# Performance work log

Measured on AMD Instinct MI355X. Metric: run time of the kernel, lower is better.

Reference implementation:

```python
import jax, jax.numpy as jnp
import numpy as np

B, L, D, H = 2, 2048, 1024, 16
HD = D // H
ROPE_BASE = 10000.0


def _chain_info(lengths):
    """lengths: [B, L] int, chain lengths packed at the front, zeros after.
    Returns per-position within-chain positions (RoPE resets per chain),
    chain ids, and a validity mask."""
    def one(row):
        csum = jnp.cumsum(row)                      # [L]
        total = csum[-1]
        p = jnp.arange(L)
        cid = jnp.searchsorted(csum, p, side='right')  # chain id per position
        prev = jnp.where(cid > 0, csum[jnp.clip(cid - 1, 0, L - 1)], 0)
        valid = p < total
        pos = jnp.where(valid, p - prev, 0).astype(jnp.float32)
        return pos, cid, valid
    return jax.vmap(one)(lengths)


def _rope_tables(pos):
    # pos: [B, L] float -> cos/sin [B, L, 1, HD]
    inv_freq = 1.0 / (ROPE_BASE ** (jnp.arange(0, HD, 2, dtype=jnp.float32) / HD))
    freqs = pos[..., None] * inv_freq               # [B, L, HD/2]
    emb = jnp.concatenate([freqs, freqs], axis=-1)  # [B, L, HD]
    return jnp.cos(emb)[:, :, None, :], jnp.sin(emb)[:, :, None, :]


def _apply_rope(x, cos, sin):
    d = x.shape[-1]
    x1, x2 = x[..., : d // 2], x[..., d // 2:]
    return x * cos + jnp.concatenate([-x2, x1], axis=-1) * sin


def _branch(x, Wqkv, bqkv, cos, sin, allowed):
    # x: [B, L, D]; allowed: [B, L, L] bool attention mask for this branch
    qkv = x @ Wqkv.T + bqkv                          # [B, L, 3D]
    qkv = qkv.reshape(B, L, 3, H, HD)
    q, k, v = qkv[:, :, 0], qkv[:, :, 1], qkv[:, :, 2]
    q = q * (HD ** -0.5)
    q = _apply_rope(q, cos, sin)
    k = _apply_rope(k, cos, sin)
    scores = jnp.einsum('bthd,bshd->bhts', q, k)     # [B, H, L, L]
    scores = jnp.where(allowed[:, None], scores, -jnp.inf)
    probs = jax.nn.softmax(scores, axis=-1)
    probs = jnp.where(jnp.isnan(probs), 0.0, probs)  # fully-masked rows -> 0
    out = jnp.einsum('bhts,bshd->bthd', probs, v)    # [B, L, H, HD]
    return out.reshape(B, L, D)


def setup_inputs() -> dict:
    key = jax.random.key(0)
    ks = jax.random.split(key, 7)
    s = 0.02
    lens = np.zeros((B, L), np.int64)
    lens[0, :8] = [300, 250, 200, 400, 350, 248, 150, 100]   # sum 1998
    lens[1, :6] = [512, 400, 300, 360, 276, 200]             # sum 2048
    return {
        'hidden_states': jax.random.normal(ks[0], (B, L, D), jnp.float32),
        'attention_mask_in_length': jnp.asarray(lens),
        'Wqkv_intra': jax.random.normal(ks[1], (3 * D, D), jnp.float32) * s,
        'bqkv_intra': jnp.zeros((3 * D,), jnp.float32),
        'Wqkv_inter': jax.random.normal(ks[2], (3 * D, D), jnp.float32) * s,
        'bqkv_inter': jnp.zeros((3 * D,), jnp.float32),
        'Wout': jax.random.normal(ks[3], (D, D), jnp.float32) * s,
        'bout': jnp.zeros((D,), jnp.float32),
    }


def reference(hidden_states, attention_mask_in_length, Wqkv_intra, bqkv_intra,
              Wqkv_inter, bqkv_inter, Wout, bout):
    pos, cid, valid = _chain_info(attention_mask_in_length)
    cos, sin = _rope_tables(pos)
    same_chain = cid[:, :, None] == cid[:, None, :]          # [B, L, L]
    key_valid = valid[:, None, :]                            # [B, 1, L]
    allowed_intra = same_chain & key_valid
    allowed_inter = (~same_chain) & key_valid
    out_intra = _branch(hidden_states, Wqkv_intra, bqkv_intra, cos, sin, allowed_intra)
    out_inter = _branch(hidden_states, Wqkv_inter, bqkv_inter, cos, sin, allowed_inter)
    return (out_intra + out_inter) @ Wout.T + bout
```

## Files before the change

### kernel.cpp

```cpp
#include <hip/hip_runtime.h>
#include <hip/hip_bf16.h>
#include <stdint.h>

#define B 2
#define L 2048
#define D 1024
#define H 16
#define HD 64
#define NT (L / 64)
#define NQT (L / 128)
#define INVALID_CID 0x40000000
#define BHLHD ((size_t)B * H * L * HD)

typedef __hip_bfloat16 bf16;
typedef __attribute__((ext_vector_type(8))) short short8;
typedef __attribute__((ext_vector_type(4))) float floatx4;
typedef __attribute__((ext_vector_type(4))) unsigned int uint4v;

static __device__ __forceinline__ short f2bf(float f) {
    bf16 h = __float2bfloat16(f);
    return *reinterpret_cast<short*>(&h);
}

static __device__ __forceinline__ void async_copy16(const void* g, void* l) {
    __builtin_amdgcn_global_load_lds((__attribute__((address_space(1))) void*)g,
                                     (__attribute__((address_space(3))) void*)l,
                                     16, 0, 0);
}

__global__ void chain_kernel(const int* __restrict__ lens,
                             float* __restrict__ pos, int* __restrict__ cid,
                             int4* __restrict__ tinfo)
{
    __shared__ int csum[L];
    __shared__ int cids[L];
    __shared__ int part[256];
    int b = blockIdx.x;
    int t = threadIdx.x;

    int loc[8];
    int s = 0;
    #pragma unroll
    for (int j = 0; j < 8; ++j) { s += lens[b * L + t * 8 + j]; loc[j] = s; }
    part[t] = s;
    __syncthreads();
    if (t == 0) {
        int acc = 0;
        for (int i = 0; i < 256; ++i) { int v = part[i]; part[i] = acc; acc += v; }
    }
    __syncthreads();
    int base = part[t];
    #pragma unroll
    for (int j = 0; j < 8; ++j) csum[t * 8 + j] = base + loc[j];
    __syncthreads();

    int total = csum[L - 1];
    for (int p = t; p < L; p += 256) {
        int cv;
        if (p < total) {
            int lo = 0, hi = L;
            while (lo < hi) {
                int mid = (lo + hi) >> 1;
                if (csum[mid] <= p) lo = mid + 1; else hi = mid;
            }
            int prev = (lo > 0) ? csum[lo - 1] : 0;
            pos[b * L + p] = (float)(p - prev);
            cv = lo;
        } else {
            pos[b * L + p] = 0.f;
            cv = INVALID_CID;
        }
        cids[p] = cv;
        cid[b * L + p] = cv;
    }
    __syncthreads();
    if (t < NT) {
        int mn = 0x7fffffff, mx = -1, any = 0, all = 1;
        for (int j = 0; j < 64; ++j) {
            int cv = cids[t * 64 + j];
            if (cv != INVALID_CID) { any = 1; mn = min(mn, cv); mx = max(mx, cv); }
            else all = 0;
        }
        tinfo[b * NT + t] = make_int4(mn, mx, any | (all << 1), 0);
    }
}

__global__ void rope_table(const float* __restrict__ pos, float2* __restrict__ tab)
{
    int idx = blockIdx.x * 256 + threadIdx.x;
    int j = idx & 31, l = idx >> 5;
    float invf = exp2f(-(float)j * (13.287712379549449f / 32.f));
    float ang = pos[l] * invf;
    tab[idx] = make_float2(cosf(ang), sinf(ang));
}

__global__ void cast_all(const float* __restrict__ x,  const float* __restrict__ Wi,
                         const float* __restrict__ We, const float* __restrict__ Wo,
                         bf16* __restrict__ xb, bf16* __restrict__ Wib,
                         bf16* __restrict__ Web, bf16* __restrict__ Wob)
{
    int bid = blockIdx.x;
    const float* src; bf16* dst; int base;
    if      (bid < 4096)  { src = x;  dst = xb;  base = bid; }
    else if (bid < 7168)  { src = Wi; dst = Wib; base = bid - 4096; }
    else if (bid < 10240) { src = We; dst = Web; base = bid - 7168; }
    else                  { src = Wo; dst = Wob; base = bid - 10240; }
    int i = (base * 256 + threadIdx.x) * 4;
    float4 v = *(const float4*)(src + i);
    dst[i + 0] = __float2bfloat16(v.x);
    dst[i + 1] = __float2bfloat16(v.y);
    dst[i + 2] = __float2bfloat16(v.z);
    dst[i + 3] = __float2bfloat16(v.w);
}

__global__ __launch_bounds__(256, 4) void gemm_qkv(
    const bf16* __restrict__ A, const bf16* __restrict__ Bw,
    const float* __restrict__ bi, const float* __restrict__ be,
    const float2* __restrict__ tab,
    bf16* __restrict__ Qo, bf16* __restrict__ Ko, bf16* __restrict__ Vto)
{
    __shared__ short Smem[2 * 128 * 32];
    short* As = Smem;
    short* Bs = Smem + 128 * 32;

    int tid = threadIdx.x;
    int wave = tid >> 6, lane = tid & 63;
    int i15 = lane & 15, q8 = lane >> 4;
    int wm = wave & 1, wn = wave >> 1;
    int m0 = blockIdx.y * 128, n0 = blockIdx.x * 128;
    const int K = D;

    floatx4 acc[4][4];
    #pragma unroll
    for (int mt = 0; mt < 4; ++mt)
        #pragma unroll
        for (int nt = 0; nt < 4; ++nt) acc[mt][nt] = (floatx4){0.f, 0.f, 0.f, 0.f};

    const short* gA = (const short*)A  + (size_t)(m0 + wave * 32 + (lane >> 2)) * K + (lane & 3) * 8;
    const short* gB = (const short*)Bw + (size_t)(n0 + wave * 32 + (lane >> 2)) * K + (lane & 3) * 8;
    short* lA = As + wave * 1024;
    short* lB = Bs + wave * 1024;

    for (int kt = 0; kt < K; kt += 32) {
        __syncthreads();
        async_copy16(gA + kt,          lA);
        async_copy16(gA + 16 * K + kt, lA + 512);
        async_copy16(gB + kt,          lB);
        async_copy16(gB + 16 * K + kt, lB + 512);
        __syncthreads();

        short8 af[4], bfr[4];
        #pragma unroll
        for (int mt = 0; mt < 4; ++mt)
            af[mt] = *(const short8*)&As[(wm * 64 + mt * 16 + i15) * 32 + q8 * 8];
        #pragma unroll
        for (int nt = 0; nt < 4; ++nt)
            bfr[nt] = *(const short8*)&Bs[(wn * 64 + nt * 16 + i15) * 32 + q8 * 8];
        #pragma unroll
        for (int mt = 0; mt < 4; ++mt)
            #pragma unroll
            for (int nt = 0; nt < 4; ++nt)
                acc[mt][nt] = __builtin_amdgcn_mfma_f32_16x16x32_bf16(af[mt], bfr[nt], acc[mt][nt], 0, 0, 0);
    }

    int nb = n0 + wn * 64;
    int segw = nb >> 10;
    int br = (segw >= 3);
    int st = segw - 3 * br;
    int h = (nb >> 6) & (H - 1);
    int b = m0 >> 11;
    int lb = (m0 & (L - 1)) + wm * 64;

    float bv[4];
    #pragma unroll
    for (int nt = 0; nt < 4; ++nt) {
        int n = nb + nt * 16 + i15;
        bv[nt] = (n < 3 * D) ? bi[n] : be[n - 3 * D];
    }

    if (st != 2) {
        bf16* out = (st == 0 ? Qo : Ko) + (size_t)br * BHLHD;
        const size_t bh = (size_t)(b * H + h) * L;
        float qs = (st == 0) ? 0.18033688011111772f : 1.0f;
        #pragma unroll
        for (int mt = 0; mt < 4; ++mt) {
            #pragma unroll
            for (int rg = 0; rg < 4; ++rg) {
                int m = m0 + wm * 64 + mt * 16 + q8 * 4 + rg;
                int l = lb + mt * 16 + q8 * 4 + rg;
                float2 cs0 = tab[(size_t)m * 32 + i15];
                float2 cs1 = tab[(size_t)m * 32 + 16 + i15];
                size_t orow = (bh + l) * HD;
                #pragma unroll
                for (int nt = 0; nt < 4; ++nt) {
                    float x  = acc[mt][nt][rg] + bv[nt];
                    float pr = acc[mt][nt ^ 2][rg] + bv[nt ^ 2];
                    float cc = (nt & 1) ? cs1.x : cs0.x;
                    float ss = (nt & 1) ? cs1.y : cs0.y;
                    float v = qs * (x * cc + ((nt < 2) ? -pr : pr) * ss);
                    out[orow + nt * 16 + i15] = __float2bfloat16(v);
                }
            }
        }
    } else {
        bf16* out = Vto + (size_t)br * BHLHD;
        const size_t bhd = (size_t)(b * H + h) * HD;
        __syncthreads();
        short* vts = Smem + wave * 64 * 20;
        #pragma unroll
        for (int mt = 0; mt < 4; ++mt) {
            #pragma unroll
            for (int nt = 0; nt < 4; ++nt) {
                uint2 w;
                w.x = (unsigned)(unsigned short)f2bf(acc[mt][nt][0] + bv[nt]) |
                      ((unsigned)(unsigned short)f2bf(acc[mt][nt][1] + bv[nt]) << 16);
                w.y = (unsigned)(unsigned short)f2bf(acc[mt][nt][2] + bv[nt]) |
                      ((unsigned)(unsigned short)f2bf(acc[mt][nt][3] + bv[nt]) << 16);
                *(uint2*)&vts[(nt * 16 + i15) * 20 + q8 * 4] = w;
            }
            uint2 r0 = *(const uint2*)&vts[lane * 20 + 0];
            uint2 r1 = *(const uint2*)&vts[lane * 20 + 4];
            uint2 r2 = *(const uint2*)&vts[lane * 20 + 8];
            uint2 r3 = *(const uint2*)&vts[lane * 20 + 12];
            size_t ga = (bhd + lane) * L + lb + mt * 16;
            uint4v v0 = (uint4v){r0.x, r0.y, r1.x, r1.y};
            uint4v v1 = (uint4v){r2.x, r2.y, r3.x, r3.y};
            *(uint4v*)&out[ga]     = v0;
            *(uint4v*)&out[ga + 8] = v1;
        }
    }
}

__global__ __launch_bounds__(256, 4) void gemm128(
    const bf16* __restrict__ A, const bf16* __restrict__ Bw,
    const float* __restrict__ bias, void* __restrict__ Cout,
    int M, int N, int K, int c_bf16)
{
    __shared__ short As[128 * 32];
    __shared__ short Bs[128 * 32];

    int tid = threadIdx.x;
    int wave = tid >> 6, lane = tid & 63;
    int i15 = lane & 15, q8 = lane >> 4;
    int wm = wave & 1, wn = wave >> 1;
    int m0 = blockIdx.y * 128, n0 = blockIdx.x * 128;

    floatx4 acc[4][4];
    #pragma unroll
    for (int mt = 0; mt < 4; ++mt)
        #pragma unroll
        for (int nt = 0; nt < 4; ++nt) acc[mt][nt] = (floatx4){0.f, 0.f, 0.f, 0.f};

    const short* gA = (const short*)A  + (size_t)(m0 + wave * 32 + (lane >> 2)) * K + (lane & 3) * 8;
    const short* gB = (const short*)Bw + (size_t)(n0 + wave * 32 + (lane >> 2)) * K + (lane & 3) * 8;
    short* lA = As + wave * 1024;
    short* lB = Bs + wave * 1024;

    for (int kt = 0; kt < K; kt += 32) {
        __syncthreads();
        async_copy16(gA + kt,          lA);
        async_copy16(gA + 16 * K + kt, lA + 512);
        async_copy16(gB + kt,          lB);
        async_copy16(gB + 16 * K + kt, lB + 512);
        __syncthreads();

        short8 af[4], bfr[4];
        #pragma unroll
        for (int mt = 0; mt < 4; ++mt)
            af[mt] = *(const short8*)&As[(wm * 64 + mt * 16 + i15) * 32 + q8 * 8];
        #pragma unroll
        for (int nt = 0; nt < 4; ++nt)
            bfr[nt] = *(const short8*)&Bs[(wn * 64 + nt * 16 + i15) * 32 + q8 * 8];
        #pragma unroll
        for (int mt = 0; mt < 4; ++mt)
            #pragma unroll
            for (int nt = 0; nt < 4; ++nt)
                acc[mt][nt] = __builtin_amdgcn_mfma_f32_16x16x32_bf16(af[mt], bfr[nt], acc[mt][nt], 0, 0, 0);
    }

    #pragma unroll
    for (int nt = 0; nt < 4; ++nt) {
        int n = n0 + wn * 64 + nt * 16 + i15;
        float bv = bias[n];
        #pragma unroll
        for (int mt = 0; mt < 4; ++mt) {
            #pragma unroll
            for (int rg = 0; rg < 4; ++rg) {
                int m = m0 + wm * 64 + mt * 16 + q8 * 4 + rg;
                float v = acc[mt][nt][rg] + bv;
                if (c_bf16) ((bf16*)Cout)[(size_t)m * N + n] = __float2bfloat16(v);
                else        ((float*)Cout)[(size_t)m * N + n] = v;
            }
        }
    }
}

__global__ __launch_bounds__(256, 2) void attn7(
    const bf16* __restrict__ Qg, const bf16* __restrict__ Kgg, const bf16* __restrict__ Vtgg,
    const int* __restrict__ cid, const int4* __restrict__ tinfo,
    bf16* __restrict__ Out)
{
    __shared__ short Ks[2][64][72];
    __shared__ short Vs[2][64][72];
    __shared__ int cls0_s[NT], cls1_s[NT];
    __shared__ int list_s[2][NT];
    __shared__ int nlist_s[2];

    int tid = threadIdx.x;
    int wave = tid >> 6, lane = tid & 63;
    int i15 = lane & 15, q8 = lane >> 4;
    int workid = ((blockIdx.x & 7) << 6) | (blockIdx.x >> 3);
    int qt = workid & (NQT - 1);
    int h  = (workid >> 4) & (H - 1);
    int b  = workid >> 8;
    int q0 = qt * 128;
    const size_t bh  = (size_t)(b * H + h) * L;
    const size_t bhd = (size_t)(b * H + h) * HD;

    int cq[2];
    #pragma unroll
    for (int g = 0; g < 2; ++g)
        cq[g] = cid[b * L + q0 + g * 64 + wave * 16 + i15];

    int4 qa = tinfo[b * NT + 2 * qt];
    int4 qb4 = tinfo[b * NT + 2 * qt + 1];
    int4 qinf;
    qinf.x = min(qa.x, qb4.x);
    qinf.y = max(qa.y, qb4.y);
    qinf.z = ((qa.z | qb4.z) & 1) | (qa.z & qb4.z & 2);
    int qall = (qinf.z >> 1) & 1;

    if (tid < NT) {
        int4 ki = tinfo[b * NT + tid];
        int kany = ki.z & 1, kall = (ki.z >> 1) & 1;
        bool disjoint = (ki.x > qinf.y) || (ki.y < qinf.x);
        bool mono = qall && kall && (qinf.x == qinf.y) && (ki.x == ki.y) && (qinf.x == ki.x);
        cls0_s[tid] = (!kany || disjoint) ? 0 : (mono ? 2 : 1);
        cls1_s[tid] = (!kany || mono) ? 0 : ((kall && disjoint) ? 2 : 1);
    }
    __syncthreads();
    if (tid < 2) {
        const int* cls = tid ? cls1_s : cls0_s;
        int n = 0;
        for (int t = 0; t < NT; ++t) {
            int c = cls[t];
            if (c) list_s[tid][n++] = (t * 64) | ((c == 2) << 16);
        }
        nlist_s[tid] = n;
    }
    __syncthreads();

    int r = tid >> 2, ccol = (tid & 3) * 16;
    int sr = ((((r >> 2) & 1) | ((r >> 5) << 1)) << 4) | (((r >> 3) & 3) << 2) | (r & 3);

    floatx4 accO[2][2][4];
    #pragma unroll
    for (int br = 0; br < 2; ++br)
        #pragma unroll
        for (int g = 0; g < 2; ++g)
            #pragma unroll
            for (int t = 0; t < 4; ++t) accO[br][g][t] = (floatx4){0.f, 0.f, 0.f, 0.f};
    float lsum[2][2] = {{0.f, 0.f}, {0.f, 0.f}};

    #pragma unroll
    for (int br = 0; br < 2; ++br) {
        const short* Qb    = (const short*)Qg  + (size_t)br * BHLHD;
        const short* Kbase = (const short*)Kgg + (size_t)br * BHLHD + (bh + r) * HD + ccol;
        const short* Vbase = (const short*)Vtgg + (size_t)br * BHLHD + (bhd + r) * L + ccol;
        int n = nlist_s[br];

        short8 qf[2][2];
        #pragma unroll
        for (int g = 0; g < 2; ++g) {
            const short* qp = Qb + (bh + q0 + g * 64 + wave * 16 + i15) * HD + q8 * 8;
            qf[g][0] = *(const short8*)(qp);
            qf[g][1] = *(const short8*)(qp + 32);
        }

        int4 pk0, pk1, pv0, pv1;
        int cur = 0;
        if (n > 0) {
            cur = list_s[br][0];
            int kt0 = cur & 0xffff;
            pk0 = *(const int4*)(Kbase + (size_t)kt0 * HD);
            pk1 = *(const int4*)(Kbase + (size_t)kt0 * HD + 8);
            pv0 = *(const int4*)(Vbase + kt0);
            pv1 = *(const int4*)(Vbase + kt0 + 8);
        }
        __syncthreads();

        for (int i = 0; i < n; ++i) {
            int kt = cur & 0xffff, full = cur >> 16;
            int buf = i & 1;

            *(int4*)&Ks[buf][sr][ccol]     = pk0;
            *(int4*)&Ks[buf][sr][ccol + 8] = pk1;
            *(int4*)&Vs[buf][r][ccol]      = pv0;
            *(int4*)&Vs[buf][r][ccol + 8]  = pv1;
            __syncthreads();

            if (i + 1 < n) {
                cur = list_s[br][i + 1];
                int nk = cur & 0xffff;
                pk0 = *(const int4*)(Kbase + (size_t)nk * HD);
                pk1 = *(const int4*)(Kbase + (size_t)nk * HD + 8);
                pv0 = *(const int4*)(Vbase + nk);
                pv1 = *(const int4*)(Vbase + nk + 8);
            }

            unsigned int dl[2][4], dh[2][4];
            #pragma unroll
            for (int t = 0; t < 4; ++t) {
                short8 b0 = *(const short8*)&Ks[buf][t * 16 + i15][q8 * 8];
                short8 b1 = *(const short8*)&Ks[buf][t * 16 + i15][32 + q8 * 8];

                floatx4 accS[2];
                #pragma unroll
                for (int g = 0; g < 2; ++g) {
                    accS[g] = (floatx4){0.f, 0.f, 0.f, 0.f};
                    accS[g] = __builtin_amdgcn_mfma_f32_16x16x32_bf16(b0, qf[g][0], accS[g], 0, 0, 0);
                    accS[g] = __builtin_amdgcn_mfma_f32_16x16x32_bf16(b1, qf[g][1], accS[g], 0, 0, 0);
                }

                if (!full) {
                    int4 ck4 = *(const int4*)(cid + b * L + kt + (q8 << 3) + ((t & 1) << 2) + ((t >> 1) << 5));
                    int ckr[4] = {ck4.x, ck4.y, ck4.z, ck4.w};
                    #pragma unroll
                    for (int g = 0; g < 2; ++g)
                        #pragma unroll
                        for (int rg = 0; rg < 4; ++rg) {
                            bool kv = (ckr[rg] != INVALID_CID);
                            bool match = (cq[g] == ckr[rg]);
                            bool ok = kv && (br ? !match : match);
                            accS[g][rg] = ok ? accS[g][rg] : -1e30f;
                        }
                }

                #pragma unroll
                for (int g = 0; g < 2; ++g) {
                    float p0 = __builtin_amdgcn_exp2f(accS[g][0]);
                    float p1 = __builtin_amdgcn_exp2f(accS[g][1]);
                    float p2 = __builtin_amdgcn_exp2f(accS[g][2]);
                    float p3 = __builtin_amdgcn_exp2f(accS[g][3]);
                    lsum[br][g] += (p0 + p1) + (p2 + p3);
                    dl[g][t] = (unsigned)(unsigned short)f2bf(p0) | ((unsigned)(unsigned short)f2bf(p1) << 16);
                    dh[g][t] = (unsigned)(unsigned short)f2bf(p2) | ((unsigned)(unsigned short)f2bf(p3) << 16);
                }
            }

            union { uint4v u; short8 s; } pa0[2], pa1[2];
            #pragma unroll
            for (int g = 0; g < 2; ++g) {
                pa0[g].u = (uint4v){dl[g][0], dh[g][0], dl[g][1], dh[g][1]};
                pa1[g].u = (uint4v){dl[g][2], dh[g][2], dl[g][3], dh[g][3]};
            }

            #pragma unroll
            for (int dt = 0; dt < 4; ++dt) {
                short8 vf0 = *(const short8*)&Vs[buf][dt * 16 + i15][q8 * 8];
                short8 vf1 = *(const short8*)&Vs[buf][dt * 16 + i15][32 + q8 * 8];
                #pragma unroll
                for (int g = 0; g < 2; ++g) {
                    accO[br][g][dt] = __builtin_amdgcn_mfma_f32_16x16x32_bf16(pa0[g].s, vf0, accO[br][g][dt], 0, 0, 0);
                    accO[br][g][dt] = __builtin_amdgcn_mfma_f32_16x16x32_bf16(pa1[g].s, vf1, accO[br][g][dt], 0, 0, 0);
                }
            }
        }
    }

    float inv[2][2][4];
    #pragma unroll
    for (int br = 0; br < 2; ++br)
        #pragma unroll
        for (int g = 0; g < 2; ++g) {
            float ls = lsum[br][g];
            ls += __shfl_xor(ls, 16, 64);
            ls += __shfl_xor(ls, 32, 64);
            #pragma unroll
            for (int rg = 0; rg < 4; ++rg) {
                float lv = __shfl(ls, q8 * 4 + rg, 64);
                inv[br][g][rg] = (lv > 0.f) ? 1.f / lv : 0.f;
            }
        }

    #pragma unroll
    for (int g = 0; g < 2; ++g)
        #pragma unroll
        for (int t = 0; t < 4; ++t)
            #pragma unroll
            for (int rg = 0; rg < 4; ++rg) {
                size_t idx = (size_t)(b * L + q0 + g * 64 + wave * 16 + q8 * 4 + rg) * D + h * HD + t * 16 + i15;
                float o = accO[0][g][t][rg] * inv[0][g][rg] + accO[1][g][t][rg] * inv[1][g][rg];
                Out[idx] = __float2bfloat16(o);
            }
}

extern "C" void kernel_launch(void* const* d_in, const int* in_sizes, int n_in,
                              void* d_out, int out_size, void* d_ws, size_t ws_size,
                              hipStream_t stream)
{
    const float* x    = (const float*)d_in[0];
    const int*   mlen = (const int*)  d_in[1];
    const float* Wi   = (const float*)d_in[2];
    const float* bi   = (const float*)d_in[3];
    const float* We   = (const float*)d_in[4];
    const float* be   = (const float*)d_in[5];
    const float* Wo   = (const float*)d_in[6];
    const float* bo   = (const float*)d_in[7];

    char* ws = (char*)d_ws;
    size_t off = 0;
    auto alloc = [&](size_t bytes) {
        void* p = ws + off;
        off += (bytes + 255) & ~(size_t)255;
        return p;
    };
    bf16*  x_b   = (bf16*) alloc((size_t)B * L * D * 2);
    bf16*  Wi_b  = (bf16*) alloc((size_t)3 * D * D * 2);
    bf16*  We_b  = (bf16*) alloc((size_t)3 * D * D * 2);
    bf16*  Wo_b  = (bf16*) alloc((size_t)D * D * 2);
    bf16*  q_b   = (bf16*) alloc(2 * BHLHD * 2);
    bf16*  k_b   = (bf16*) alloc(2 * BHLHD * 2);
    bf16*  vt_b  = (bf16*) alloc(2 * BHLHD * 2);
    bf16*  sum_b = (bf16*) alloc((size_t)B * L * D * 2);
    float* pos   = (float*)alloc((size_t)B * L * 4);
    int*   cid   = (int*)  alloc((size_t)B * L * 4);
    int4*  tinfo = (int4*) alloc((size_t)B * NT * 16);
    float2* rtab = (float2*)alloc((size_t)B * L * 32 * 8);
    (void)ws_size; (void)n_in; (void)in_sizes; (void)out_size;

    chain_kernel<<<B, 256, 0, stream>>>(mlen, pos, cid, tinfo);
    rope_table<<<B * L * 32 / 256, 256, 0, stream>>>(pos, rtab);

    cast_all<<<11264, 256, 0, stream>>>(x, Wi, We, Wo, x_b, Wi_b, We_b, Wo_b);

    dim3 gq(6 * D / 128, B * L / 128);
    gemm_qkv<<<gq, 256, 0, stream>>>(x_b, Wi_b, bi, be, rtab, q_b, k_b, vt_b);

    attn7<<<B * H * NQT, 256, 0, stream>>>(q_b, k_b, vt_b, cid, tinfo, sum_b);

    dim3 go(D / 128, B * L / 128);
    gemm128<<<go, 256, 0, stream>>>(sum_b, Wo_b, bo, d_out, B * L, D, D, 0);
}
```

Before: 290.1 us.

## Halve attention query tile to 64 rows, doubling blocks and raising occupancy

The attention kernel now processes 64 query rows per block instead of 128. The grid becomes 1024 blocks and launch bounds allow 4 blocks per CU. The tile-classification lists are computed per 64-row tile, so a block skips more key tiles when its chain range is narrower. The aim is better load balance and latency hiding from more resident waves. The cost is that each K/V tile loaded into LDS is reused by half as many query rows, which doubles total K/V load traffic.

```diff
diff --git a/kernel.cpp b/kernel.cpp
--- a/kernel.cpp
+++ b/kernel.cpp
@@ -8,7 +8,6 @@
 #define H 16
 #define HD 64
 #define NT (L / 64)
-#define NQT (L / 128)
 #define INVALID_CID 0x40000000
 #define BHLHD ((size_t)B * H * L * HD)
 
@@ -295,7 +294,7 @@
     }
 }
 
-__global__ __launch_bounds__(256, 2) void attn7(
+__global__ __launch_bounds__(256, 4) void attn9(
     const bf16* __restrict__ Qg, const bf16* __restrict__ Kgg, const bf16* __restrict__ Vtgg,
     const int* __restrict__ cid, const int4* __restrict__ tinfo,
     bf16* __restrict__ Out)
@@ -309,25 +308,17 @@
     int tid = threadIdx.x;
     int wave = tid >> 6, lane = tid & 63;
     int i15 = lane & 15, q8 = lane >> 4;
-    int workid = ((blockIdx.x & 7) << 6) | (blockIdx.x >> 3);
-    int qt = workid & (NQT - 1);
-    int h  = (workid >> 4) & (H - 1);
-    int b  = workid >> 8;
-    int q0 = qt * 128;
+    int workid = ((blockIdx.x & 7) << 7) | (blockIdx.x >> 3);
+    int qt = workid & (NT - 1);
+    int h  = (workid >> 5) & (H - 1);
+    int b  = workid >> 9;
+    int q0 = qt * 64;
     const size_t bh  = (size_t)(b * H + h) * L;
     const size_t bhd = (size_t)(b * H + h) * HD;
 
-    int cq[2];
-    #pragma unroll
-    for (int g = 0; g < 2; ++g)
-        cq[g] = cid[b * L + q0 + g * 64 + wave * 16 + i15];
-
-    int4 qa = tinfo[b * NT + 2 * qt];
-    int4 qb4 = tinfo[b * NT + 2 * qt + 1];
-    int4 qinf;
-    qinf.x = min(qa.x, qb4.x);
-    qinf.y = max(qa.y, qb4.y);
-    qinf.z = ((qa.z | qb4.z) & 1) | (qa.z & qb4.z & 2);
+    int cq = cid[b * L + q0 + wave * 16 + i15];
+
+    int4 qinf = tinfo[b * NT + qt];
     int qall = (qinf.z >> 1) & 1;
 
     if (tid < NT) {
@@ -353,28 +344,25 @@
     int r = tid >> 2, ccol = (tid & 3) * 16;
     int sr = ((((r >> 2) & 1) | ((r >> 5) << 1)) << 4) | (((r >> 3) & 3) << 2) | (r & 3);
 
-    floatx4 accO[2][2][4];
+    floatx4 accO[2][4];
     #pragma unroll
     for (int br = 0; br < 2; ++br)
         #pragma unroll
-        for (int g = 0; g < 2; ++g)
-            #pragma unroll
-            for (int t = 0; t < 4; ++t) accO[br][g][t] = (floatx4){0.f, 0.f, 0.f, 0.f};
-    float lsum[2][2] = {{0.f, 0.f}, {0.f, 0.f}};
+        for (int t = 0; t < 4; ++t) accO[br][t] = (floatx4){0.f, 0.f, 0.f, 0.f};
+    float lsum[2] = {0.f, 0.f};
 
     #pragma unroll
     for (int br = 0; br < 2; ++br) {
-        const short* Qb    = (const short*)Qg  + (size_t)br * BHLHD;
-        const short* Kbase = (const short*)Kgg + (size_t)br * BHLHD + (bh + r) * HD + ccol;
+        const short* Qb    = (const short*)Qg   + (size_t)br * BHLHD;
+        const short* Kbase = (const short*)Kgg  + (size_t)br * BHLHD + (bh + r) * HD + ccol;
         const short* Vbase = (const short*)Vtgg + (size_t)br * BHLHD + (bhd + r) * L + ccol;
         int n = nlist_s[br];
 
-        short8 qf[2][2];
-        #pragma unroll
-        for (int g = 0; g < 2; ++g) {
-            const short* qp = Qb + (bh + q0 + g * 64 + wave * 16 + i15) * HD + q8 * 8;
-            qf[g][0] = *(const short8*)(qp);
-            qf[g][1] = *(const short8*)(qp + 32);
+        short8 qf0, qf1;
+        {
+            const short* qp = Qb + (bh + q0 + wave * 16 + i15) * HD + q8 * 8;
+            qf0 = *(const short8*)(qp);
+            qf1 = *(const short8*)(qp + 32);
         }
 
         int4 pk0, pk1, pv0, pv1;
@@ -408,91 +396,72 @@
                 pv1 = *(const int4*)(Vbase + nk + 8);
             }
 
-            unsigned int dl[2][4], dh[2][4];
+            unsigned int dl[4], dh[4];
             #pragma unroll
             for (int t = 0; t < 4; ++t) {
                 short8 b0 = *(const short8*)&Ks[buf][t * 16 + i15][q8 * 8];
                 short8 b1 = *(const short8*)&Ks[buf][t * 16 + i15][32 + q8 * 8];
 
-                floatx4 accS[2];
-                #pragma unroll
-                for (int g = 0; g < 2; ++g) {
-                    accS[g] = (floatx4){0.f, 0.f, 0.f, 0.f};
-                    accS[g] = __builtin_amdgcn_mfma_f32_16x16x32_bf16(b0, qf[g][0], accS[g], 0, 0, 0);
-                    accS[g] = __builtin_amdgcn_mfma_f32_16x16x32_bf16(b1, qf[g][1], accS[g], 0, 0, 0);
-                }
+                floatx4 accS = (floatx4){0.f, 0.f, 0.f, 0.f};
+                accS = __builtin_amdgcn_mfma_f32_16x16x32_bf16(b0, qf0, accS, 0, 0, 0);
+                accS = __builtin_amdgcn_mfma_f32_16x16x32_bf16(b1, qf1, accS, 0, 0, 0);
 
                 if (!full) {
                     int4 ck4 = *(const int4*)(cid + b * L + kt + (q8 << 3) + ((t & 1) << 2) + ((t >> 1) << 5));
                     int ckr[4] = {ck4.x, ck4.y, ck4.z, ck4.w};
                     #pragma unroll
-                    for (int g = 0; g < 2; ++g)
-                        #pragma unroll
-                        for (int rg = 0; rg < 4; ++rg) {
-                            bool kv = (ckr[rg] != INVALID_CID);
-                            bool match = (cq[g] == ckr[rg]);
-                            bool ok = kv && (br ? !match : match);
-                            accS[g][rg] = ok ? accS[g][rg] : -1e30f;
-                        }
+                    for (int rg = 0; rg < 4; ++rg) {
+                        bool kv = (ckr[rg] != INVALID_CID);
+                        bool match = (cq == ckr[rg]);
+                        bool ok = kv && (br ? !match : match);
+                        accS[rg] = ok ? accS[rg] : -1e30f;
+                    }
                 }
 
-                #pragma unroll
-                for (int g = 0; g < 2; ++g) {
-                    float p0 = __builtin_amdgcn_exp2f(accS[g][0]);
-                    float p1 = __builtin_amdgcn_exp2f(accS[g][1]);
-                    float p2 = __builtin_amdgcn_exp2f(accS[g][2]);
-                    float p3 = __builtin_amdgcn_exp2f(accS[g][3]);
-                    lsum[br][g] += (p0 + p1) + (p2 + p3);
-                    dl[g][t] = (unsigned)(unsigned short)f2bf(p0) | ((unsigned)(unsigned short)f2bf(p1) << 16);
-                    dh[g][t] = (unsigned)(unsigned short)f2bf(p2) | ((unsigned)(unsigned short)f2bf(p3) << 16);
-                }
-            }
-
-            union { uint4v u; short8 s; } pa0[2], pa1[2];
-            #pragma unroll
-            for (int g = 0; g < 2; ++g) {
-                pa0[g].u = (uint4v){dl[g][0], dh[g][0], dl[g][1], dh[g][1]};
-                pa1[g].u = (uint4v){dl[g][2], dh[g][2], dl[g][3], dh[g][3]};
-            }
+                float p0 = __builtin_amdgcn_exp2f(accS[0]);
+                float p1 = __builtin_amdgcn_exp2f(accS[1]);
+                float p2 = __builtin_amdgcn_exp2f(accS[2]);
+                float p3 = __builtin_amdgcn_exp2f(accS[3]);
+                lsum[br] += (p0 + p1) + (p2 + p3);
+                dl[t] = (unsigned)(unsigned short)f2bf(p0) | ((unsigned)(unsigned short)f2bf(p1) << 16);
+                dh[t] = (unsigned)(unsigned short)f2bf(p2) | ((unsigned)(unsigned short)f2bf(p3) << 16);
+            }
+
+            union { uint4v u; short8 s; } pa0, pa1;
+            pa0.u = (uint4v){dl[0], dh[0], dl[1], dh[1]};
+            pa1.u = (uint4v){dl[2], dh[2], dl[3], dh[3]};
 
             #pragma unroll
             for (int dt = 0; dt < 4; ++dt) {
                 short8 vf0 = *(const short8*)&Vs[buf][dt * 16 + i15][q8 * 8];
                 short8 vf1 = *(const short8*)&Vs[buf][dt * 16 + i15][32 + q8 * 8];
-                #pragma unroll
-                for (int g = 0; g < 2; ++g) {
-                    accO[br][g][dt] = __builtin_amdgcn_mfma_f32_16x16x32_bf16(pa0[g].s, vf0, accO[br][g][dt], 0, 0, 0);
-                    accO[br][g][dt] = __builtin_amdgcn_mfma_f32_16x16x32_bf16(pa1[g].s, vf1, accO[br][g][dt], 0, 0, 0);
-                }
-            }
-        }
-    }
-
-    float inv[2][2][4];
-    #pragma unroll
-    for (int br = 0; br < 2; ++br)
-        #pragma unroll
-        for (int g = 0; g < 2; ++g) {
-            float ls = lsum[br][g];
-            ls += __shfl_xor(ls, 16, 64);
-            ls += __shfl_xor(ls, 32, 64);
-            #pragma unroll
-            for (int rg = 0; rg < 4; ++rg) {
-                float lv = __shfl(ls, q8 * 4 + rg, 64);
-                inv[br][g][rg] = (lv > 0.f) ? 1.f / lv : 0.f;
-            }
-        }
-
-    #pragma unroll
-    for (int g = 0; g < 2; ++g)
-        #pragma unroll
-        for (int t = 0; t < 4; ++t)
-            #pragma unroll
-            for (int rg = 0; rg < 4; ++rg) {
-                size_t idx = (size_t)(b * L + q0 + g * 64 + wave * 16 + q8 * 4 + rg) * D + h * HD + t * 16 + i15;
-                float o = accO[0][g][t][rg] * inv[0][g][rg] + accO[1][g][t][rg] * inv[1][g][rg];
-                Out[idx] = __float2bfloat16(o);
-            }
+                accO[br][dt] = __builtin_amdgcn_mfma_f32_16x16x32_bf16(pa0.s, vf0, accO[br][dt], 0, 0, 0);
+                accO[br][dt] = __builtin_amdgcn_mfma_f32_16x16x32_bf16(pa1.s, vf1, accO[br][dt], 0, 0, 0);
+            }
+        }
+    }
+
+    float inv[2][4];
+    #pragma unroll
+    for (int br = 0; br < 2; ++br) {
+        float ls = lsum[br];
+        ls += __shfl_xor(ls, 16, 64);
+        ls += __shfl_xor(ls, 32, 64);
+        #pragma unroll
+        for (int rg = 0; rg < 4; ++rg) {
+            float lv = __shfl(ls, q8 * 4 + rg, 64);
+            inv[br][rg] = (lv > 0.f) ? 1.f / lv : 0.f;
+        }
+    }
+
+    #pragma unroll
+    for (int t = 0; t < 4; ++t)
+        #pragma unroll
+        for (int rg = 0; rg < 4; ++rg) {
+            size_t idx = (size_t)(b * L + q0 + wave * 16 + q8 * 4 + rg) * D + h * HD + t * 16 + i15;
+            float o = accO[0][t][rg] * inv[0][rg] + accO[1][t][rg] * inv[1][rg];
+            Out[idx] = __float2bfloat16(o);
+        }
 }
 
 extern "C" void kernel_launch(void* const* d_in, const int* in_sizes, int n_in,
@@ -537,7 +506,7 @@
     dim3 gq(6 * D / 128, B * L / 128);
     gemm_qkv<<<gq, 256, 0, stream>>>(x_b, Wi_b, bi, be, rtab, q_b, k_b, vt_b);
 
-    attn7<<<B * H * NQT, 256, 0, stream>>>(q_b, k_b, vt_b, cid, tinfo, sum_b);
+    attn9<<<B * H * NT, 256, 0, stream>>>(q_b, k_b, vt_b, cid, tinfo, sum_b);
 
     dim3 go(D / 128, B * L / 128);
     gemm128<<<go, 256, 0, stream>>>(sum_b, Wo_b, bo, d_out, B * L, D, D, 0);
```

Result: no change. 293.2 us (+1.1%).
